# Kernel optimization log

Hardware: AMD Instinct MI355X
Metric: run time of the kernel (lower is better)

The kernel has to match this reference:

```python
import jax, jax.numpy as jnp
import numpy as np
import math

B, CPLX, D_CNT, F_BINS, T_BINS = 8, 2, 16, 512, 256


def _dft_mats(F):
    r = np.arange(F)
    phase = -2.0 * math.pi * (r[None, :] * r[:, None]) / F
    return jnp.asarray(np.cos(phase), jnp.float32), jnp.asarray(np.sin(phase), jnp.float32)


def setup_inputs() -> dict:
    key = jax.random.key(0)
    kx, k1, k2, k3, k4 = jax.random.split(key, 5)
    x = jax.random.normal(kx, (B, CPLX, D_CNT, F_BINS, T_BINS), dtype=jnp.float32)
    W1 = jax.random.normal(k1, (F_BINS, F_BINS), dtype=jnp.float32) * 0.02
    b1 = jax.random.normal(k2, (F_BINS,), dtype=jnp.float32) * 0.02
    W2 = jax.random.normal(k3, (F_BINS, F_BINS), dtype=jnp.float32) * 0.02
    b2 = jax.random.normal(k4, (F_BINS,), dtype=jnp.float32) * 0.02
    return {"x": x, "W1": W1, "b1": b1, "W2": W2, "b2": b2}


def _dft(z, COS, SIN):
    # z: [B, 2, D, T, F]; matmul broadcasts over (B, D, T)
    re, im = z[:, 0], z[:, 1]
    return jnp.stack((re @ COS - im @ SIN, re @ SIN + im @ COS), axis=1)


def _idft(z, COS, SIN, F):
    re, im = z[:, 0], z[:, 1]
    return jnp.stack(((re @ COS + im @ SIN) / F, (im @ COS - re @ SIN) / F), axis=1)


def _mul_complex(a, b):
    h1 = a * b
    ret_real = h1[:, 0] - h1[:, 1]
    h2 = a * jnp.flip(b, axis=1)
    ret_imag = h2[:, 0] + h2[:, 1]
    return jnp.stack((ret_real, ret_imag), axis=1)


def reference(x, W1, b1, W2, b2):
    F = x.shape[3]
    COS, SIN = _dft_mats(F)
    h = jnp.transpose(x, (0, 1, 2, 4, 3))  # [B,2,D,T,F]
    w = h @ W1.T + b1
    w = w @ W2.T + b2
    w = jax.nn.softmax(w, axis=-1)
    x_ifft = _idft(h, COS, SIN, F)
    y_ifft = _idft(w, COS, SIN, F)
    h2 = F * _dft(_mul_complex(x_ifft, y_ifft), COS, SIN)
    return jnp.transpose(h2, (0, 1, 2, 4, 3))
```

## Files before the change

### kernel.cpp

```cpp
#include <hip/hip_runtime.h>
#include <math.h>

#define FB 512
#define TB 256
#define PLANE (FB * TB)
typedef long long i64;
typedef _Float16 f16;
typedef _Float16 f16x8 __attribute__((ext_vector_type(8)));
typedef _Float16 f16x4 __attribute__((ext_vector_type(4)));
typedef float f32x4 __attribute__((ext_vector_type(4)));

#define MFMA16(a, b, c) __builtin_amdgcn_mfma_f32_16x16x32_f16(a, b, c, 0, 0, 0)

__device__ __forceinline__ void tcvt_tile(const float* __restrict__ src,
                                          f16* __restrict__ dst,
                                          int sstride, int dstride,
                                          int r0, int c0, int tid,
                                          float (*ld)[65]) {
    const int lrr = tid >> 4, lc = (tid & 15) * 4;
    f32x4 v0 = *(const f32x4*)&src[(i64)(r0 + lrr + 0) * sstride + c0 + lc];
    f32x4 v1 = *(const f32x4*)&src[(i64)(r0 + lrr + 16) * sstride + c0 + lc];
    f32x4 v2 = *(const f32x4*)&src[(i64)(r0 + lrr + 32) * sstride + c0 + lc];
    f32x4 v3 = *(const f32x4*)&src[(i64)(r0 + lrr + 48) * sstride + c0 + lc];
#pragma unroll
    for (int j = 0; j < 4; ++j) {
        ld[lrr + 0][lc + j] = v0[j];
        ld[lrr + 16][lc + j] = v1[j];
        ld[lrr + 32][lc + j] = v2[j];
        ld[lrr + 48][lc + j] = v3[j];
    }
    __syncthreads();
    const int tr2 = tid >> 3, fc = (tid & 7) * 8;
#pragma unroll
    for (int pass = 0; pass < 2; ++pass) {
        const int t = tr2 + pass * 32;
        f16x8 o;
#pragma unroll
        for (int j = 0; j < 8; ++j) o[j] = (f16)ld[fc + j][t];
        *(f16x8*)&dst[(i64)(c0 + t) * dstride + r0 + fc] = o;
    }
}

__global__ __launch_bounds__(256) void k_pre2(const float* __restrict__ X,
                                              f16* __restrict__ O,
                                              const float* __restrict__ W1,
                                              f16* __restrict__ W1t,
                                              const float* __restrict__ W2,
                                              f16* __restrict__ W2h,
                                              float* __restrict__ zrs,
                                              const float* __restrict__ b1,
                                              const float* __restrict__ b2,
                                              float* __restrict__ beff) {
    __shared__ float ld[64][65];
    const int bid = blockIdx.x;
    const int tid = threadIdx.x;
    if (bid < 8192) {
        const int p = bid >> 5;
        const int f0 = ((bid >> 2) & 7) * 64, t0 = (bid & 3) * 64;
        tcvt_tile(X + (i64)p * PLANE, O + (i64)p * PLANE, TB, FB, f0, t0, tid, ld);
    } else if (bid < 8256) {
        const int w = bid - 8192;
        tcvt_tile(W1, W1t, FB, FB, (w >> 3) * 64, (w & 7) * 64, tid, ld);
    } else if (bid < 8384) {
        const i64 idx = ((i64)(bid - 8256) * 256 + tid) * 8;
        const float4 a = *(const float4*)&W2[idx];
        const float4 b = *(const float4*)&W2[idx + 4];
        f16x8 o;
        o[0] = (f16)a.x; o[1] = (f16)a.y; o[2] = (f16)a.z; o[3] = (f16)a.w;
        o[4] = (f16)b.x; o[5] = (f16)b.y; o[6] = (f16)b.z; o[7] = (f16)b.w;
        *(f16x8*)&W2h[idx] = o;
    } else if (bid == 8384) {
        zrs[tid] = 0.f;
        zrs[tid + 256] = 0.f;
    } else {
        const int m = (bid - 8385) * 4 + (tid >> 6);
        const int lane = tid & 63;
        const float* w2r = W2 + (i64)m * FB + lane * 8;
        const f32x4 a0 = *(const f32x4*)(w2r);
        const f32x4 a1 = *(const f32x4*)(w2r + 4);
        const f32x4 c0 = *(const f32x4*)(b1 + lane * 8);
        const f32x4 c1 = *(const f32x4*)(b1 + lane * 8 + 4);
        float acc = 0.f;
#pragma unroll
        for (int j = 0; j < 4; ++j) acc = fmaf(a0[j], c0[j], acc);
#pragma unroll
        for (int j = 0; j < 4; ++j) acc = fmaf(a1[j], c1[j], acc);
#pragma unroll
        for (int o = 32; o > 0; o >>= 1) acc += __shfl_xor(acc, o);
        if (lane == 0) beff[m] = acc + b2[m];
    }
}

__global__ __launch_bounds__(256, 2) void k_rgemm(const f16* __restrict__ A,
                                                  const f16* __restrict__ In,
                                                  const float* __restrict__ bias,
                                                  f16* __restrict__ Out) {
    __shared__ f16 Asx[128][40], Bsx[128][40];
    const int slab = blockIdx.z;
    const f16* Bsrc = In + (i64)slab * PLANE;
    f16* Odst = Out + (i64)slab * PLANE;
    const int t0 = blockIdx.x * 128, m0 = blockIdx.y * 128;
    const int tid = threadIdx.x;
    const int wave = tid >> 6, lane = tid & 63;
    const int wm = wave >> 1, wn = wave & 1;
    const int lr = lane & 15, lg = lane >> 4;
    const int srow = tid >> 2, sgrp = (tid & 3) * 8;

    f32x4 acc[4][4] = {};
    f16x8 nA[2], nB[2];
#pragma unroll
    for (int i = 0; i < 2; ++i) {
        const int row = i * 64 + srow;
        nA[i] = *(const f16x8*)(A + (i64)(m0 + row) * FB + sgrp);
        nB[i] = *(const f16x8*)(Bsrc + (i64)(t0 + row) * FB + sgrp);
    }
#pragma unroll
    for (int i = 0; i < 2; ++i) {
        const int row = i * 64 + srow;
        *(f16x8*)&Asx[row][sgrp] = nA[i];
        *(f16x8*)&Bsx[row][sgrp] = nB[i];
    }
    __syncthreads();

#pragma unroll 1
    for (int kt = 0; kt < 16; ++kt) {
        if (kt < 15) {
            const int k0 = (kt + 1) * 32;
#pragma unroll
            for (int i = 0; i < 2; ++i) {
                const int row = i * 64 + srow;
                nA[i] = *(const f16x8*)(A + (i64)(m0 + row) * FB + k0 + sgrp);
                nB[i] = *(const f16x8*)(Bsrc + (i64)(t0 + row) * FB + k0 + sgrp);
            }
        }
        f16x8 aA[4], bB[4];
#pragma unroll
        for (int mf = 0; mf < 4; ++mf)
            aA[mf] = *(const f16x8*)&Asx[wm * 64 + mf * 16 + lr][lg * 8];
#pragma unroll
        for (int nf = 0; nf < 4; ++nf)
            bB[nf] = *(const f16x8*)&Bsx[wn * 64 + nf * 16 + lr][lg * 8];
#pragma unroll
        for (int nf = 0; nf < 4; ++nf)
#pragma unroll
            for (int mf = 0; mf < 4; ++mf)
                acc[mf][nf] = MFMA16(aA[mf], bB[nf], acc[mf][nf]);
        __syncthreads();
        if (kt < 15) {
#pragma unroll
            for (int i = 0; i < 2; ++i) {
                const int row = i * 64 + srow;
                *(f16x8*)&Asx[row][sgrp] = nA[i];
                *(f16x8*)&Bsx[row][sgrp] = nB[i];
            }
        }
        __syncthreads();
    }

#pragma unroll
    for (int mf = 0; mf < 4; ++mf) {
        const int m = m0 + wm * 64 + mf * 16 + lg * 4;
        const float4 bv = *(const float4*)&bias[m];
        const float bb[4] = {bv.x, bv.y, bv.z, bv.w};
#pragma unroll
        for (int nf = 0; nf < 4; ++nf) {
            const int t = t0 + wn * 64 + nf * 16 + lr;
            f16x4 o;
#pragma unroll
            for (int r = 0; r < 4; ++r) o[r] = (f16)(acc[mf][nf][r] + bb[r]);
            *(f16x4*)&Odst[(i64)t * FB + m] = o;
        }
    }
}


#define TWO_PI_OVER_512 0.012271846303085129f
#define TWO_PI_OVER_64 0.0981747704246810387f
#define R2C 0.70710678118654752f

template <int SGN>
__device__ __forceinline__ void fft8(float xr[8], float xi[8]) {
    const float sg = (float)SGN;
    float t0r = xr[0] + xr[4], t0i = xi[0] + xi[4];
    float u0r = xr[0] - xr[4], u0i = xi[0] - xi[4];
    float t1r = xr[1] + xr[5], t1i = xi[1] + xi[5];
    float d1r = xr[1] - xr[5], d1i = xi[1] - xi[5];
    float u1r = R2C * (d1r - sg * d1i), u1i = R2C * (sg * d1r + d1i);
    float t2r = xr[2] + xr[6], t2i = xi[2] + xi[6];
    float d2r = xr[2] - xr[6], d2i = xi[2] - xi[6];
    float u2r = -sg * d2i, u2i = sg * d2r;
    float t3r = xr[3] + xr[7], t3i = xi[3] + xi[7];
    float d3r = xr[3] - xr[7], d3i = xi[3] - xi[7];
    float u3r = -R2C * (d3r + sg * d3i), u3i = R2C * (sg * d3r - d3i);
    float p0r = t0r + t2r, p0i = t0i + t2i, q0r = t0r - t2r, q0i = t0i - t2i;
    float p1r = t1r + t3r, p1i = t1i + t3i;
    float q1r = -sg * (t1i - t3i), q1i = sg * (t1r - t3r);
    float p2r = u0r + u2r, p2i = u0i + u2i, q2r = u0r - u2r, q2i = u0i - u2i;
    float p3r = u1r + u3r, p3i = u1i + u3i;
    float q3r = -sg * (u1i - u3i), q3i = sg * (u1r - u3r);
    xr[0] = p0r + p1r; xi[0] = p0i + p1i;
    xr[4] = p0r - p1r; xi[4] = p0i - p1i;
    xr[2] = q0r + q1r; xi[2] = q0i + q1i;
    xr[6] = q0r - q1r; xi[6] = q0i - q1i;
    xr[1] = p2r + p3r; xi[1] = p2i + p3i;
    xr[5] = p2r - p3r; xi[5] = p2i - p3i;
    xr[3] = q2r + q3r; xi[3] = q2i + q3i;
    xr[7] = q2r - q3r; xi[7] = q2i - q3i;
}

template <int SGN>
__device__ __forceinline__ void fft512x2(float ar[8], float ai[8],
                                         float br[8], float bi[8], int lane,
                                         float4* __restrict__ L,
                                         const float w1c[7], const float w1s[7],
                                         const float w2c[7], const float w2s[7]) {
    const float sg = (float)SGN;
    fft8<SGN>(ar, ai);
    fft8<SGN>(br, bi);
#pragma unroll
    for (int m = 1; m < 8; ++m) {
        const float wc = w1c[m - 1], ws = sg * w1s[m - 1];
        float tr = ar[m], ti = ai[m];
        ar[m] = tr * wc - ti * ws; ai[m] = tr * ws + ti * wc;
        tr = br[m]; ti = bi[m];
        br[m] = tr * wc - ti * ws; bi[m] = tr * ws + ti * wc;
    }
#pragma unroll
    for (int m = 0; m < 8; ++m)
        L[lane * 9 + m] = make_float4(ar[m], ai[m], br[m], bi[m]);
    {
        const int a8 = lane & 7, m8 = lane >> 3;
#pragma unroll
        for (int b8 = 0; b8 < 8; ++b8) {
            const float4 v = L[(a8 + 8 * b8) * 9 + m8];
            ar[b8] = v.x; ai[b8] = v.y; br[b8] = v.z; bi[b8] = v.w;
        }
    }
    fft8<SGN>(ar, ai);
    fft8<SGN>(br, bi);
#pragma unroll
    for (int n = 1; n < 8; ++n) {
        const float wc = w2c[n - 1], ws = sg * w2s[n - 1];
        float tr = ar[n], ti = ai[n];
        ar[n] = tr * wc - ti * ws; ai[n] = tr * ws + ti * wc;
        tr = br[n]; ti = bi[n];
        br[n] = tr * wc - ti * ws; bi[n] = tr * ws + ti * wc;
    }
    {
        const int a2 = lane & 7, m2 = lane >> 3;
#pragma unroll
        for (int n = 0; n < 8; ++n)
            L[(m2 + 8 * n) * 9 + a2] = make_float4(ar[n], ai[n], br[n], bi[n]);
    }
#pragma unroll
    for (int j = 0; j < 8; ++j) {
        const float4 v = L[lane * 9 + j];
        ar[j] = v.x; ai[j] = v.y; br[j] = v.z; bi[j] = v.w;
    }
    fft8<SGN>(ar, ai);
    fft8<SGN>(br, bi);
}

__device__ __forceinline__ float wave_max(float v) {
#pragma unroll
    for (int m = 1; m <= 32; m <<= 1) v = fmaxf(v, __shfl_xor(v, m));
    return v;
}
__device__ __forceinline__ float wave_sum(float v) {
#pragma unroll
    for (int m = 1; m <= 32; m <<= 1) v += __shfl_xor(v, m);
    return v;
}

__device__ __forceinline__ void softmax8(float w[8]) {
    float mx = w[0];
#pragma unroll
    for (int j = 1; j < 8; ++j) mx = fmaxf(mx, w[j]);
    mx = wave_max(mx);
    float sm = 0.f;
#pragma unroll
    for (int j = 0; j < 8; ++j) { w[j] = __expf(w[j] - mx); sm += w[j]; }
    sm = wave_sum(sm);
    const float inv = 1.0f / sm;
#pragma unroll
    for (int j = 0; j < 8; ++j) w[j] *= inv;
}

__device__ __forceinline__ void load_marshal(const f16* __restrict__ Hre,
                                             const f16* __restrict__ Him,
                                             const f16* __restrict__ Wre,
                                             const f16* __restrict__ Wim,
                                             i64 rowbase, int lane,
                                             float4* __restrict__ L,
                                             float hr[8], float hi2[8],
                                             float wr[8], float wi[8]) {
    const f16x8 vhr = *(const f16x8*)(Hre + rowbase + 8 * lane);
    const f16x8 vhi = *(const f16x8*)(Him + rowbase + 8 * lane);
    const f16x8 vwr = *(const f16x8*)(Wre + rowbase + 8 * lane);
    const f16x8 vwi = *(const f16x8*)(Wim + rowbase + 8 * lane);
#pragma unroll
    for (int j = 0; j < 8; ++j)
        L[lane * 9 + j] = make_float4((float)vhr[j], (float)vhi[j],
                                      (float)vwr[j], (float)vwi[j]);
    const int c = lane >> 3, q = lane & 7;
#pragma unroll
    for (int v = 0; v < 8; ++v) {
        const float4 f4 = L[(8 * v + c) * 9 + q];
        hr[v] = f4.x; hi2[v] = f4.y; wr[v] = f4.z; wi[v] = f4.w;
    }
}

__device__ __forceinline__ void fftconv_block(const f16* __restrict__ xh,
                                              const f16* __restrict__ logits,
                                              f16* __restrict__ conv,
                                              int tblk, int cs, int chunkoff,
                                              int wave, int lane, float4* L) {
    const int b = cs >> 4, d = cs & 15;
    const int pre = b * 32 + d;
    const int pim = pre + 16;

    float w1c[7], w1s[7], w2c[7], w2s[7];
    {
        float s1, c1;
        __sincosf((float)lane * TWO_PI_OVER_512, &s1, &c1);
        w1c[0] = c1; w1s[0] = s1;
#pragma unroll
        for (int m = 1; m < 7; ++m) {
            const float pc = w1c[m - 1], ps = w1s[m - 1];
            w1c[m] = pc * c1 - ps * s1;
            w1s[m] = pc * s1 + ps * c1;
        }
        float s2, c2;
        __sincosf((float)(lane & 7) * TWO_PI_OVER_64, &s2, &c2);
        w2c[0] = c2; w2s[0] = s2;
#pragma unroll
        for (int n = 1; n < 7; ++n) {
            const float pc = w2c[n - 1], ps = w2s[n - 1];
            w2c[n] = pc * c2 - ps * s2;
            w2s[n] = pc * s2 + ps * c2;
        }
    }

    const f16* Hre = xh + (i64)pre * PLANE;
    const f16* Him = xh + (i64)pim * PLANE;
    const f16* Wre = logits + (i64)pre * PLANE;
    const f16* Wim = logits + (i64)pim * PLANE;
    f16* Cre = conv + (i64)(pre - chunkoff) * PLANE;
    f16* Cim = conv + (i64)(pim - chunkoff) * PLANE;

    const int t1a = tblk * 8 + wave * 2;

    float p0r[8], p0i[8], p1r[8], p1i[8];
    {
        float hr[8], hi2[8], wr[8], wi[8];
        load_marshal(Hre, Him, Wre, Wim, (i64)t1a * FB, lane, L, hr, hi2, wr, wi);
        softmax8(wr);
        softmax8(wi);
        fft512x2<1>(hr, hi2, wr, wi, lane, L, w1c, w1s, w2c, w2s);
#pragma unroll
        for (int j = 0; j < 8; ++j) {
            p0r[j] = (hr[j] * wr[j] - hi2[j] * wi[j]) * (1.0f / 512.0f);
            p0i[j] = (hr[j] * wi[j] + hi2[j] * wr[j]) * (1.0f / 512.0f);
        }
    }
    {
        float hr[8], hi2[8], wr[8], wi[8];
        load_marshal(Hre, Him, Wre, Wim, (i64)(t1a + 1) * FB, lane, L, hr, hi2, wr, wi);
        softmax8(wr);
        softmax8(wi);
        fft512x2<1>(hr, hi2, wr, wi, lane, L, w1c, w1s, w2c, w2s);
#pragma unroll
        for (int j = 0; j < 8; ++j) {
            p1r[j] = (hr[j] * wr[j] - hi2[j] * wi[j]) * (1.0f / 512.0f);
            p1i[j] = (hr[j] * wi[j] + hi2[j] * wr[j]) * (1.0f / 512.0f);
        }
    }
    fft512x2<-1>(p0r, p0i, p1r, p1i, lane, L, w1c, w1s, w2c, w2s);

    {
        const int a = lane & 7, bq = lane >> 3;
#pragma unroll
        for (int s = 0; s < 8; ++s)
            L[(bq + 8 * s) * 9 + a] = make_float4(p0r[s], p0i[s], p1r[s], p1i[s]);
    }
    f16x8 o0r, o0i, o1r, o1i;
#pragma unroll
    for (int j = 0; j < 8; ++j) {
        const float4 g = L[lane * 9 + j];
        o0r[j] = (f16)g.x; o0i[j] = (f16)g.y;
        o1r[j] = (f16)g.z; o1i[j] = (f16)g.w;
    }
    *(f16x8*)(Cre + (i64)t1a * FB + 8 * lane) = o0r;
    *(f16x8*)(Cim + (i64)t1a * FB + 8 * lane) = o0i;
    *(f16x8*)(Cre + (i64)(t1a + 1) * FB + 8 * lane) = o1r;
    *(f16x8*)(Cim + (i64)(t1a + 1) * FB + 8 * lane) = o1i;
}

__device__ __forceinline__ void transpose_block(const f16* __restrict__ C,
                                                float* __restrict__ O,
                                                int tb, int fb, int p, int pbase,
                                                int tid, float (*ld)[65]) {
    const f16* src = C + (i64)p * PLANE;
    float* dst = O + (i64)(p + pbase) * PLANE;
    const int t0 = tb * 64, f0 = fb * 64;
    const int tr = tid >> 3, fc = (tid & 7) * 8;
    f16x8 u0 = *(const f16x8*)&src[(i64)(t0 + tr) * FB + f0 + fc];
    f16x8 u1 = *(const f16x8*)&src[(i64)(t0 + tr + 32) * FB + f0 + fc];
#pragma unroll
    for (int j = 0; j < 8; ++j) {
        ld[fc + j][tr] = (float)u0[j];
        ld[fc + j][tr + 32] = (float)u1[j];
    }
    __syncthreads();
    const int fr = tid >> 4, tc = (tid & 15) * 4;
#pragma unroll
    for (int i = 0; i < 4; ++i) {
        const int f = fr + i * 16;
        float4 o;
        o.x = ld[f][tc + 0]; o.y = ld[f][tc + 1];
        o.z = ld[f][tc + 2]; o.w = ld[f][tc + 3];
        *(float4*)&dst[(i64)(f0 + f) * TB + t0 + tc] = o;
    }
}

__global__ __launch_bounds__(256, 2) void k_fftconv(const f16* __restrict__ xh,
                                                    const f16* __restrict__ logits,
                                                    f16* __restrict__ conv,
                                                    int csbase, int chunkoff) {
    __shared__ float4 LDS[4][576];
    const int wave = threadIdx.x >> 6, lane = threadIdx.x & 63;
    fftconv_block(xh, logits, conv, blockIdx.x, blockIdx.y + csbase, chunkoff,
                  wave, lane, LDS[wave]);
}

__global__ __launch_bounds__(256, 2) void k_mid(const f16* __restrict__ xh,
                                                const f16* __restrict__ logits,
                                                f16* __restrict__ conv1,
                                                const f16* __restrict__ conv0,
                                                float* __restrict__ out) {
    __shared__ __align__(16) char raw[36864];
    const int bid = blockIdx.x;
    const int tid = threadIdx.x;
    if (bid < 2048) {
        const int wave = tid >> 6, lane = tid & 63;
        float4* L = (float4*)raw + wave * 576;
        fftconv_block(xh, logits, conv1, bid & 31, 64 + (bid >> 5), 128, wave, lane, L);
    } else {
        const int w = bid - 2048;
        float (*ld)[65] = (float(*)[65])raw;
        transpose_block(conv0, out, w & 3, (w >> 2) & 7, w >> 5, 0, tid, ld);
    }
}

__global__ __launch_bounds__(256) void k_transpose_out(const f16* __restrict__ C,
                                                       float* __restrict__ O,
                                                       int pbase) {
    __shared__ float ld[64][65];
    transpose_block(C, O, blockIdx.x, blockIdx.y, blockIdx.z, pbase, threadIdx.x, ld);
}

extern "C" void kernel_launch(void* const* d_in, const int* in_sizes, int n_in,
                              void* d_out, int out_size, void* d_ws, size_t ws_size,
                              hipStream_t stream) {
    (void)in_sizes; (void)n_in; (void)out_size; (void)ws_size;
    const float* x = (const float*)d_in[0];
    const float* W1 = (const float*)d_in[1];
    const float* b1 = (const float*)d_in[2];
    const float* W2 = (const float*)d_in[3];
    const float* b2 = (const float*)d_in[4];
    float* out = (float*)d_out;

    char* ws = (char*)d_ws;
    const i64 TENB = (i64)67108864;
    const i64 HALFB = (i64)33554432;
    f16* Weff  = (f16*)(ws);
    float* beff = (float*)(ws + 524288);
    f16* W1t  = (f16*)(ws + 528384);
    f16* W2h  = (f16*)(ws + 1052672);
    float* zrs = (float*)(ws + 1576960);
    f16* xh     = (f16*)(ws + 1581056);
    f16* logits = (f16*)(ws + 1581056 + TENB);
    f16* conv0  = (f16*)(ws + 1581056 + 2 * TENB);
    f16* conv1  = (f16*)(ws + 1581056 + 2 * TENB + HALFB);

    k_pre2<<<dim3(8513), dim3(256), 0, stream>>>(x, xh, W1, W1t, W2, W2h, zrs, b1, b2, beff);
    k_rgemm<<<dim3(4, 4, 1), dim3(256), 0, stream>>>(W1t, W2h, zrs, Weff);
    k_rgemm<<<dim3(TB / 128, FB / 128, 256), dim3(256), 0, stream>>>(Weff, xh, beff, logits);
    k_fftconv<<<dim3(32, 64), dim3(256), 0, stream>>>(xh, logits, conv0, 0, 0);
    k_mid<<<dim3(6144), dim3(256), 0, stream>>>(xh, logits, conv1, conv0, out);
    k_transpose_out<<<dim3(4, 8, 128), dim3(256), 0, stream>>>(conv1, out, 128);
}
```

Measured before the change: 227.5 us.

## Swizzle GEMM and FFT-conv blocks across XCDs and drop overlapped mid kernel

The big logits GEMM becomes a 1D grid whose block ids are remapped so that consecutive slabs land on the same XCD, aiming to improve L2 reuse of the shared Weff operand and input slabs. The FFT-conv is merged into a single launch with an XCD-aware mapping over channel slabs. The previous split schedule, which overlapped the second half of the FFT-conv with the transpose of the first half in one fused kernel, is removed in favour of one transpose launch over all planes. This trades away cross-stage overlap for better cache locality and fewer launches.

New measurement: 220.9 us. 2.9% less time.

```diff
diff --git a/kernel.cpp b/kernel.cpp
--- a/kernel.cpp
+++ b/kernel.cpp
@@ -91,86 +91,106 @@
     }
 }
 
+__device__ __forceinline__ void rgemm_body(const f16* __restrict__ A,
+                                           const f16* __restrict__ In,
+                                           const float* __restrict__ bias,
+                                           f16* __restrict__ Out,
+                                           int t0, int m0, int slab,
+                                           f16 (*Asx)[40], f16 (*Bsx)[40]) {
+    const f16* Bsrc = In + (i64)slab * PLANE;
+    f16* Odst = Out + (i64)slab * PLANE;
+    const int tid = threadIdx.x;
+    const int wave = tid >> 6, lane = tid & 63;
+    const int wm = wave >> 1, wn = wave & 1;
+    const int lr = lane & 15, lg = lane >> 4;
+    const int srow = tid >> 2, sgrp = (tid & 3) * 8;
+
+    f32x4 acc[4][4] = {};
+    f16x8 nA[2], nB[2];
+#pragma unroll
+    for (int i = 0; i < 2; ++i) {
+        const int row = i * 64 + srow;
+        nA[i] = *(const f16x8*)(A + (i64)(m0 + row) * FB + sgrp);
+        nB[i] = *(const f16x8*)(Bsrc + (i64)(t0 + row) * FB + sgrp);
+    }
+#pragma unroll
+    for (int i = 0; i < 2; ++i) {
+        const int row = i * 64 + srow;
+        *(f16x8*)&Asx[row][sgrp] = nA[i];
+        *(f16x8*)&Bsx[row][sgrp] = nB[i];
+    }
+    __syncthreads();
+
+#pragma unroll 1
+    for (int kt = 0; kt < 16; ++kt) {
+        if (kt < 15) {
+            const int k0 = (kt + 1) * 32;
+#pragma unroll
+            for (int i = 0; i < 2; ++i) {
+                const int row = i * 64 + srow;
+                nA[i] = *(const f16x8*)(A + (i64)(m0 + row) * FB + k0 + sgrp);
+                nB[i] = *(const f16x8*)(Bsrc + (i64)(t0 + row) * FB + k0 + sgrp);
+            }
+        }
+        f16x8 aA[4], bB[4];
+#pragma unroll
+        for (int mf = 0; mf < 4; ++mf)
+            aA[mf] = *(const f16x8*)&Asx[wm * 64 + mf * 16 + lr][lg * 8];
+#pragma unroll
+        for (int nf = 0; nf < 4; ++nf)
+            bB[nf] = *(const f16x8*)&Bsx[wn * 64 + nf * 16 + lr][lg * 8];
+#pragma unroll
+        for (int nf = 0; nf < 4; ++nf)
+#pragma unroll
+            for (int mf = 0; mf < 4; ++mf)
+                acc[mf][nf] = MFMA16(aA[mf], bB[nf], acc[mf][nf]);
+        __syncthreads();
+        if (kt < 15) {
+#pragma unroll
+            for (int i = 0; i < 2; ++i) {
+                const int row = i * 64 + srow;
+                *(f16x8*)&Asx[row][sgrp] = nA[i];
+                *(f16x8*)&Bsx[row][sgrp] = nB[i];
+            }
+        }
+        __syncthreads();
+    }
+
+#pragma unroll
+    for (int mf = 0; mf < 4; ++mf) {
+        const int m = m0 + wm * 64 + mf * 16 + lg * 4;
+        const float4 bv = *(const float4*)&bias[m];
+        const float bb[4] = {bv.x, bv.y, bv.z, bv.w};
+#pragma unroll
+        for (int nf = 0; nf < 4; ++nf) {
+            const int t = t0 + wn * 64 + nf * 16 + lr;
+            f16x4 o;
+#pragma unroll
+            for (int r = 0; r < 4; ++r) o[r] = (f16)(acc[mf][nf][r] + bb[r]);
+            *(f16x4*)&Odst[(i64)t * FB + m] = o;
+        }
+    }
+}
+
 __global__ __launch_bounds__(256, 2) void k_rgemm(const f16* __restrict__ A,
                                                   const f16* __restrict__ In,
                                                   const float* __restrict__ bias,
                                                   f16* __restrict__ Out) {
     __shared__ f16 Asx[128][40], Bsx[128][40];
-    const int slab = blockIdx.z;
-    const f16* Bsrc = In + (i64)slab * PLANE;
-    f16* Odst = Out + (i64)slab * PLANE;
-    const int t0 = blockIdx.x * 128, m0 = blockIdx.y * 128;
-    const int tid = threadIdx.x;
-    const int wave = tid >> 6, lane = tid & 63;
-    const int wm = wave >> 1, wn = wave & 1;
-    const int lr = lane & 15, lg = lane >> 4;
-    const int srow = tid >> 2, sgrp = (tid & 3) * 8;
-
-    f32x4 acc[4][4] = {};
-    f16x8 nA[2], nB[2];
-#pragma unroll
-    for (int i = 0; i < 2; ++i) {
-        const int row = i * 64 + srow;
-        nA[i] = *(const f16x8*)(A + (i64)(m0 + row) * FB + sgrp);
-        nB[i] = *(const f16x8*)(Bsrc + (i64)(t0 + row) * FB + sgrp);
-    }
-#pragma unroll
-    for (int i = 0; i < 2; ++i) {
-        const int row = i * 64 + srow;
-        *(f16x8*)&Asx[row][sgrp] = nA[i];
-        *(f16x8*)&Bsx[row][sgrp] = nB[i];
-    }
-    __syncthreads();
-
-#pragma unroll 1
-    for (int kt = 0; kt < 16; ++kt) {
-        if (kt < 15) {
-            const int k0 = (kt + 1) * 32;
-#pragma unroll
-            for (int i = 0; i < 2; ++i) {
-                const int row = i * 64 + srow;
-                nA[i] = *(const f16x8*)(A + (i64)(m0 + row) * FB + k0 + sgrp);
-                nB[i] = *(const f16x8*)(Bsrc + (i64)(t0 + row) * FB + k0 + sgrp);
-            }
-        }
-        f16x8 aA[4], bB[4];
-#pragma unroll
-        for (int mf = 0; mf < 4; ++mf)
-            aA[mf] = *(const f16x8*)&Asx[wm * 64 + mf * 16 + lr][lg * 8];
-#pragma unroll
-        for (int nf = 0; nf < 4; ++nf)
-            bB[nf] = *(const f16x8*)&Bsx[wn * 64 + nf * 16 + lr][lg * 8];
-#pragma unroll
-        for (int nf = 0; nf < 4; ++nf)
-#pragma unroll
-            for (int mf = 0; mf < 4; ++mf)
-                acc[mf][nf] = MFMA16(aA[mf], bB[nf], acc[mf][nf]);
-        __syncthreads();
-        if (kt < 15) {
-#pragma unroll
-            for (int i = 0; i < 2; ++i) {
-                const int row = i * 64 + srow;
-                *(f16x8*)&Asx[row][sgrp] = nA[i];
-                *(f16x8*)&Bsx[row][sgrp] = nB[i];
-            }
-        }
-        __syncthreads();
-    }
-
-#pragma unroll
-    for (int mf = 0; mf < 4; ++mf) {
-        const int m = m0 + wm * 64 + mf * 16 + lg * 4;
-        const float4 bv = *(const float4*)&bias[m];
-        const float bb[4] = {bv.x, bv.y, bv.z, bv.w};
-#pragma unroll
-        for (int nf = 0; nf < 4; ++nf) {
-            const int t = t0 + wn * 64 + nf * 16 + lr;
-            f16x4 o;
-#pragma unroll
-            for (int r = 0; r < 4; ++r) o[r] = (f16)(acc[mf][nf][r] + bb[r]);
-            *(f16x4*)&Odst[(i64)t * FB + m] = o;
-        }
-    }
+    rgemm_body(A, In, bias, Out, blockIdx.x * 128, blockIdx.y * 128, blockIdx.z,
+               Asx, Bsx);
+}
+
+__global__ __launch_bounds__(256, 2) void k_rgemm_swz(const f16* __restrict__ A,
+                                                      const f16* __restrict__ In,
+                                                      const float* __restrict__ bias,
+                                                      f16* __restrict__ Out) {
+    __shared__ f16 Asx[128][40], Bsx[128][40];
+    const int id = blockIdx.x;
+    const int xcd = id & 7, q = id >> 3;
+    const int m = q & 3;
+    const int G = ((q >> 2) << 3) | xcd;
+    rgemm_body(A, In, bias, Out, (G & 1) * 128, m * 128, G >> 1, Asx, Bsx);
 }
 
 
@@ -313,7 +333,7 @@
 __device__ __forceinline__ void fftconv_block(const f16* __restrict__ xh,
                                               const f16* __restrict__ logits,
                                               f16* __restrict__ conv,
-                                              int tblk, int cs, int chunkoff,
+                                              int tblk, int cs,
                                               int wave, int lane, float4* L) {
     const int b = cs >> 4, d = cs & 15;
     const int pre = b * 32 + d;
@@ -345,8 +365,8 @@
     const f16* Him = xh + (i64)pim * PLANE;
     const f16* Wre = logits + (i64)pre * PLANE;
     const f16* Wim = logits + (i64)pim * PLANE;
-    f16* Cre = conv + (i64)(pre - chunkoff) * PLANE;
-    f16* Cim = conv + (i64)(pim - chunkoff) * PLANE;
+    f16* Cre = conv + (i64)pre * PLANE;
+    f16* Cim = conv + (i64)pim * PLANE;
 
     const int t1a = tblk * 8 + wave * 2;
 
@@ -396,13 +416,26 @@
     *(f16x8*)(Cim + (i64)(t1a + 1) * FB + 8 * lane) = o1i;
 }
 
-__device__ __forceinline__ void transpose_block(const f16* __restrict__ C,
-                                                float* __restrict__ O,
-                                                int tb, int fb, int p, int pbase,
-                                                int tid, float (*ld)[65]) {
+__global__ __launch_bounds__(256, 2) void k_fftconv_all(const f16* __restrict__ xh,
+                                                        const f16* __restrict__ logits,
+                                                        f16* __restrict__ conv) {
+    __shared__ float4 LDS[4][576];
+    const int id = blockIdx.x;
+    const int xcd = id & 7, r = id >> 3;
+    const int tblk = r & 31;
+    const int cs = (xcd << 4) | (r >> 5);
+    const int wave = threadIdx.x >> 6, lane = threadIdx.x & 63;
+    fftconv_block(xh, logits, conv, tblk, cs, wave, lane, LDS[wave]);
+}
+
+__global__ __launch_bounds__(256) void k_transpose_out(const f16* __restrict__ C,
+                                                       float* __restrict__ O) {
+    __shared__ float ld[64][65];
+    const int tid = threadIdx.x;
+    const int p = blockIdx.z;
     const f16* src = C + (i64)p * PLANE;
-    float* dst = O + (i64)(p + pbase) * PLANE;
-    const int t0 = tb * 64, f0 = fb * 64;
+    float* dst = O + (i64)p * PLANE;
+    const int t0 = blockIdx.x * 64, f0 = blockIdx.y * 64;
     const int tr = tid >> 3, fc = (tid & 7) * 8;
     f16x8 u0 = *(const f16x8*)&src[(i64)(t0 + tr) * FB + f0 + fc];
     f16x8 u1 = *(const f16x8*)&src[(i64)(t0 + tr + 32) * FB + f0 + fc];
@@ -421,42 +454,6 @@
         o.z = ld[f][tc + 2]; o.w = ld[f][tc + 3];
         *(float4*)&dst[(i64)(f0 + f) * TB + t0 + tc] = o;
     }
-}
-
-__global__ __launch_bounds__(256, 2) void k_fftconv(const f16* __restrict__ xh,
-                                                    const f16* __restrict__ logits,
-                                                    f16* __restrict__ conv,
-                                                    int csbase, int chunkoff) {
-    __shared__ float4 LDS[4][576];
-    const int wave = threadIdx.x >> 6, lane = threadIdx.x & 63;
-    fftconv_block(xh, logits, conv, blockIdx.x, blockIdx.y + csbase, chunkoff,
-                  wave, lane, LDS[wave]);
-}
-
-__global__ __launch_bounds__(256, 2) void k_mid(const f16* __restrict__ xh,
-                                                const f16* __restrict__ logits,
-                                                f16* __restrict__ conv1,
-                                                const f16* __restrict__ conv0,
-                                                float* __restrict__ out) {
-    __shared__ __align__(16) char raw[36864];
-    const int bid = blockIdx.x;
-    const int tid = threadIdx.x;
-    if (bid < 2048) {
-        const int wave = tid >> 6, lane = tid & 63;
-        float4* L = (float4*)raw + wave * 576;
-        fftconv_block(xh, logits, conv1, bid & 31, 64 + (bid >> 5), 128, wave, lane, L);
-    } else {
-        const int w = bid - 2048;
-        float (*ld)[65] = (float(*)[65])raw;
-        transpose_block(conv0, out, w & 3, (w >> 2) & 7, w >> 5, 0, tid, ld);
-    }
-}
-
-__global__ __launch_bounds__(256) void k_transpose_out(const f16* __restrict__ C,
-                                                       float* __restrict__ O,
-                                                       int pbase) {
-    __shared__ float ld[64][65];
-    transpose_block(C, O, blockIdx.x, blockIdx.y, blockIdx.z, pbase, threadIdx.x, ld);
 }
 
 extern "C" void kernel_launch(void* const* d_in, const int* in_sizes, int n_in,
@@ -472,7 +469,6 @@
 
     char* ws = (char*)d_ws;
     const i64 TENB = (i64)67108864;
-    const i64 HALFB = (i64)33554432;
     f16* Weff  = (f16*)(ws);
     float* beff = (float*)(ws + 524288);
     f16* W1t  = (f16*)(ws + 528384);
@@ -480,13 +476,11 @@
     float* zrs = (float*)(ws + 1576960);
     f16* xh     = (f16*)(ws + 1581056);
     f16* logits = (f16*)(ws + 1581056 + TENB);
-    f16* conv0  = (f16*)(ws + 1581056 + 2 * TENB);
-    f16* conv1  = (f16*)(ws + 1581056 + 2 * TENB + HALFB);
+    f16* conv   = (f16*)(ws + 1581056 + 2 * TENB);
 
     k_pre2<<<dim3(8513), dim3(256), 0, stream>>>(x, xh, W1, W1t, W2, W2h, zrs, b1, b2, beff);
     k_rgemm<<<dim3(4, 4, 1), dim3(256), 0, stream>>>(W1t, W2h, zrs, Weff);
-    k_rgemm<<<dim3(TB / 128, FB / 128, 256), dim3(256), 0, stream>>>(Weff, xh, beff, logits);
-    k_fftconv<<<dim3(32, 64), dim3(256), 0, stream>>>(xh, logits, conv0, 0, 0);
-    k_mid<<<dim3(6144), dim3(256), 0, stream>>>(xh, logits, conv1, conv0, out);
-    k_transpose_out<<<dim3(4, 8, 128), dim3(256), 0, stream>>>(conv1, out, 128);
-}
+    k_rgemm_swz<<<dim3(2048), dim3(256), 0, stream>>>(Weff, xh, beff, logits);
+    k_fftconv_all<<<dim3(4096), dim3(256), 0, stream>>>(xh, logits, conv);
+    k_transpose_out<<<dim3(4, 8, 256), dim3(256), 0, stream>>>(conv, out);
+}
```
